# Kernel optimization log

Measured on AMD Instinct MI355X. Metric: run time of the kernel, lower is better.

The kernel has to match this reference:

```python
import jax, jax.numpy as jnp
import numpy as np

D_MODEL = 2048
N_HEADS = 32
N_KV_HEADS = 8
HEAD_DIM = D_MODEL // N_HEADS
ROPE_BASE = 10000.0

def setup_inputs() -> dict:
    key = jax.random.key(0)
    ks = jax.random.split(key, 5)
    B, S = 1, 2048
    x = jax.random.normal(ks[0], (B, S, D_MODEL), dtype=jnp.float32)
    sc = 1.0 / np.sqrt(D_MODEL)
    Wq = jax.random.normal(ks[1], (D_MODEL, D_MODEL), dtype=jnp.float32) * sc
    Wk = jax.random.normal(ks[2], (N_KV_HEADS * HEAD_DIM, D_MODEL), dtype=jnp.float32) * sc
    Wv = jax.random.normal(ks[3], (N_KV_HEADS * HEAD_DIM, D_MODEL), dtype=jnp.float32) * sc
    Wo = jax.random.normal(ks[4], (D_MODEL, D_MODEL), dtype=jnp.float32) * sc
    return {"x": x, "Wq": Wq, "Wk": Wk, "Wv": Wv, "Wo": Wo}

def _rope_cos_sin(seq_len, dtype):
    inv_freq = 1.0 / (ROPE_BASE ** (jnp.arange(0, HEAD_DIM, 2, dtype=jnp.float32) / HEAD_DIM))
    t = jnp.arange(seq_len, dtype=jnp.float32)
    freqs = jnp.einsum('i,j->ij', t, inv_freq)          # [S, hd/2]
    emb = jnp.concatenate([freqs, freqs], axis=-1)      # [S, hd]
    return jnp.cos(emb).astype(dtype), jnp.sin(emb).astype(dtype)

def _rotate_half(x):
    x1, x2 = x[..., : HEAD_DIM // 2], x[..., HEAD_DIM // 2 :]
    return jnp.concatenate([-x2, x1], axis=-1)

def reference(x, Wq, Wk, Wv, Wo):
    B, S, _ = x.shape
    scale = HEAD_DIM ** -0.5
    # projections (Linear: x @ W.T)
    q = (x @ Wq.T).reshape(B, S, N_HEADS, HEAD_DIM).transpose(0, 2, 1, 3)      # [B,H,S,hd]
    k = (x @ Wk.T).reshape(B, S, N_KV_HEADS, HEAD_DIM).transpose(0, 2, 1, 3)   # [B,Hkv,S,hd]
    v = (x @ Wv.T).reshape(B, S, N_KV_HEADS, HEAD_DIM).transpose(0, 2, 1, 3)
    cos, sin = _rope_cos_sin(S, x.dtype)                # [S,hd], broadcasts over B,H
    q = q * cos + _rotate_half(q) * sin
    k = k * cos + _rotate_half(k) * sin
    rep = N_HEADS // N_KV_HEADS
    k = jnp.repeat(k, rep, axis=1)                       # [B,H,S,hd]
    v = jnp.repeat(v, rep, axis=1)
    scores = jnp.einsum('bhqd,bhkd->bhqk', q, k) * scale # [B,H,S,S]
    attn = jax.nn.softmax(scores, axis=-1)
    out = jnp.einsum('bhqk,bhkd->bhqd', attn, v)         # [B,H,S,hd]
    out = out.transpose(0, 2, 1, 3).reshape(B, S, D_MODEL)
    return out @ Wo.T
```

## Files before the change

### kernel.cpp

```cpp
#include <hip/hip_runtime.h>
#include <hip/hip_bf16.h>
#include <cmath>

typedef __bf16 bf16_t;
typedef __attribute__((ext_vector_type(8))) __bf16 bf16x8;
typedef __attribute__((ext_vector_type(4))) float f32x4;
typedef __attribute__((ext_vector_type(4))) short s16x4;

#define S_LEN 2048
#define DMODEL 2048
#define KVDIM 512
#define NHEADS 32
#define NKV 8
#define HDIM 64

__device__ inline f32x4 zero4() { f32x4 z; z[0]=0.f; z[1]=0.f; z[2]=0.f; z[3]=0.f; return z; }

__global__ void convert_all(const float* __restrict__ s0, bf16_t* __restrict__ d0,
                            const float* __restrict__ s1, bf16_t* __restrict__ d1,
                            const float* __restrict__ s2, bf16_t* __restrict__ d2,
                            const float* __restrict__ s3, bf16_t* __restrict__ d3,
                            const float* __restrict__ s4, bf16_t* __restrict__ d4) {
  int b = blockIdx.x;
  const float* src; bf16_t* dst; int boff;
  if      (b < 2048) { src = s0; dst = d0; boff = b; }
  else if (b < 4096) { src = s1; dst = d1; boff = b - 2048; }
  else if (b < 4608) { src = s2; dst = d2; boff = b - 4096; }
  else if (b < 5120) { src = s3; dst = d3; boff = b - 4608; }
  else               { src = s4; dst = d4; boff = b - 5120; }
  int idx = (boff * 256 + threadIdx.x) * 8;
  bf16x8 v;
#pragma unroll
  for (int j = 0; j < 8; j++) v[j] = (bf16_t)src[idx + j];
  *(bf16x8*)(dst + idx) = v;
}

template <int BN, bool F32OUT>
__device__ __forceinline__ void gemm_core(const bf16_t* __restrict__ A,
                                          const bf16_t* __restrict__ Bt,
                                          void* __restrict__ Cout,
                                          int N, int K, int bm, int bn) {
  constexpr int NT_W = BN / 32;
  __shared__ __attribute__((aligned(16))) bf16_t As[128 * 64];
  __shared__ __attribute__((aligned(16))) bf16_t Bs[BN * 64];
  const int tid  = threadIdx.x;
  const int wave = tid >> 6, lane = tid & 63;
  const int wm = wave >> 1, wn = wave & 1;
  const int quad = lane >> 4, lr = lane & 15;
  const int srow = lane >> 3, scol = lane & 7;

  f32x4 acc[4][NT_W];
#pragma unroll
  for (int i = 0; i < 4; i++)
#pragma unroll
    for (int j = 0; j < NT_W; j++) acc[i][j] = zero4();

  for (int k0 = 0; k0 < K; k0 += 64) {
#pragma unroll
    for (int i = 0; i < 4; i++) {
      const bf16_t* gA = A + (size_t)(bm + i * 32 + wave * 8 + srow) * K + k0 + scol * 8;
      bf16_t* lA = As + (i * 32 + wave * 8) * 64;
      __builtin_amdgcn_global_load_lds((const __attribute__((address_space(1))) void*)gA,
                                       (__attribute__((address_space(3))) void*)lA, 16, 0, 0);
    }
#pragma unroll
    for (int i = 0; i < BN / 32; i++) {
      const bf16_t* gB = Bt + (size_t)(bn + i * 32 + wave * 8 + srow) * K + k0 + scol * 8;
      bf16_t* lB = Bs + (i * 32 + wave * 8) * 64;
      __builtin_amdgcn_global_load_lds((const __attribute__((address_space(1))) void*)gB,
                                       (__attribute__((address_space(3))) void*)lB, 16, 0, 0);
    }
    __syncthreads();
#pragma unroll
    for (int ks = 0; ks < 2; ks++) {
      bf16x8 a[4], b[NT_W];
#pragma unroll
      for (int mt = 0; mt < 4; mt++)
        a[mt] = *(const bf16x8*)&As[(wm * 64 + mt * 16 + lr) * 64 + ks * 32 + quad * 8];
#pragma unroll
      for (int nt = 0; nt < NT_W; nt++)
        b[nt] = *(const bf16x8*)&Bs[(wn * (BN / 2) + nt * 16 + lr) * 64 + ks * 32 + quad * 8];
#pragma unroll
      for (int mt = 0; mt < 4; mt++)
#pragma unroll
        for (int nt = 0; nt < NT_W; nt++)
          acc[mt][nt] = __builtin_amdgcn_mfma_f32_16x16x32_bf16(a[mt], b[nt], acc[mt][nt], 0, 0, 0);
    }
    __syncthreads();
  }

#pragma unroll
  for (int mt = 0; mt < 4; mt++)
#pragma unroll
    for (int nt = 0; nt < NT_W; nt++)
#pragma unroll
      for (int r = 0; r < 4; r++) {
        int row = bm + wm * 64 + mt * 16 + quad * 4 + r;
        int col = bn + wn * (BN / 2) + nt * 16 + lr;
        if (F32OUT) ((float*)Cout)[(size_t)row * N + col] = acc[mt][nt][r];
        else ((bf16_t*)Cout)[(size_t)row * N + col] = (bf16_t)acc[mt][nt][r];
      }
}

__global__ __launch_bounds__(256) void gemm_proj(const bf16_t* __restrict__ xb,
                                                 const bf16_t* __restrict__ Wqb,
                                                 const bf16_t* __restrict__ Wkb,
                                                 const bf16_t* __restrict__ Wvb,
                                                 bf16_t* __restrict__ qb,
                                                 bf16_t* __restrict__ kb,
                                                 bf16_t* __restrict__ vb) {
  int b = blockIdx.x;
  if (b < 512) {
    gemm_core<64, false>(xb, Wqb, qb, 2048, 2048, (b >> 5) * 128, (b & 31) * 64);
  } else if (b < 640) {
    int r = b - 512;
    gemm_core<64, false>(xb, Wkb, kb, 512, 2048, (r >> 3) * 128, (r & 7) * 64);
  } else {
    int r = b - 640;
    gemm_core<64, false>(Wvb, xb, vb, 2048, 2048, (r >> 5) * 128, (r & 31) * 64);
  }
}

__global__ __launch_bounds__(256) void gemm_out(const bf16_t* __restrict__ A,
                                                const bf16_t* __restrict__ Bt,
                                                float* __restrict__ C) {
  int b = blockIdx.x;
  gemm_core<64, true>(A, Bt, C, 2048, 2048, (b >> 5) * 128, (b & 31) * 64);
}

__global__ void rope_k(bf16_t* __restrict__ kb) {
  int idx = blockIdx.x * 256 + threadIdx.x;
  int s = idx >> 8;
  int rem = idx & 255;
  int head = rem >> 5;
  int i = rem & 31;
  float freq = __expf(-0.2878231366f * (float)i);
  float ang = (float)s * freq;
  float sn, cs;
  sincosf(ang, &sn, &cs);
  size_t base = (size_t)s * KVDIM + head * 64 + i;
  float x0 = (float)kb[base];
  float x1 = (float)kb[base + 32];
  kb[base]      = (bf16_t)(x0 * cs - x1 * sn);
  kb[base + 32] = (bf16_t)(x1 * cs + x0 * sn);
}

__global__ __launch_bounds__(256) void attn_kernel(const bf16_t* __restrict__ q,
                                                   const bf16_t* __restrict__ k,
                                                   const bf16_t* __restrict__ vT,
                                                   bf16_t* __restrict__ out) {
  __shared__ __attribute__((aligned(16))) bf16_t Ks[128 * 64];
  __shared__ __attribute__((aligned(16))) bf16_t Vs[64 * 128];
  const int tid  = threadIdx.x;
  const int wave = tid >> 6, lane = tid & 63;
  const int quad = lane >> 4, lr = lane & 15;
  const int srow = lane >> 3, scol = lane & 7;
  const int vrow = lane >> 4, vcol = lane & 15;
  const int cg = scol ^ srow;
  const int qt = blockIdx.x, h = blockIdx.y;
  const int hkv = h >> 2;
  const int qrow0 = qt * 64 + wave * 16;
  const int sw = lr & 7;
  const int c0 = (quad ^ sw) * 8;
  const int c1 = ((quad + 4) ^ sw) * 8;

  bf16x8 aq0, aq1;
  {
    const bf16_t* qp = q + (size_t)(qrow0 + lr) * DMODEL + h * HDIM + quad * 8;
    bf16x8 r0 = *(const bf16x8*)qp;
    bf16x8 r1 = *(const bf16x8*)(qp + 32);
    float srow_f = (float)(qrow0 + lr);
#pragma unroll
    for (int j = 0; j < 8; j++) {
      float freq = __expf(-0.2878231366f * (float)(quad * 8 + j));
      float sn, cs;
      sincosf(srow_f * freq, &sn, &cs);
      float x0 = (float)r0[j], x1 = (float)r1[j];
      aq0[j] = (bf16_t)(x0 * cs - x1 * sn);
      aq1[j] = (bf16_t)(x1 * cs + x0 * sn);
    }
  }

  f32x4 O[4];
  float l_lane = 0.f;
#pragma unroll
  for (int mt = 0; mt < 4; mt++) O[mt] = zero4();

  for (int kt = 0; kt < S_LEN; kt += 128) {
#pragma unroll
    for (int j = 0; j < 4; j++) {
      const bf16_t* gK = k + (size_t)(kt + wave * 32 + j * 8 + srow) * KVDIM + hkv * HDIM + cg * 8;
      bf16_t* lK = Ks + (wave * 32 + j * 8) * 64;
      __builtin_amdgcn_global_load_lds((const __attribute__((address_space(1))) void*)gK,
                                       (__attribute__((address_space(3))) void*)lK, 16, 0, 0);
    }
#pragma unroll
    for (int j = 0; j < 4; j++) {
      int dg = wave * 16 + j * 4 + vrow;
      int cgv = vcol ^ (dg & 7);
      const bf16_t* gV = vT + (size_t)(hkv * HDIM + dg) * S_LEN + kt + cgv * 8;
      bf16_t* lV = Vs + (wave * 16 + j * 4) * 128;
      __builtin_amdgcn_global_load_lds((const __attribute__((address_space(1))) void*)gV,
                                       (__attribute__((address_space(3))) void*)lV, 16, 0, 0);
    }
    __syncthreads();

    f32x4 sc[8];
#pragma unroll
    for (int nt = 0; nt < 8; nt++) sc[nt] = zero4();
#pragma unroll
    for (int nt = 0; nt < 8; nt++) {
      const int rk = (nt * 16 + lr) * 64;
      bf16x8 kb0 = *(const bf16x8*)&Ks[rk + c0];
      bf16x8 kb1 = *(const bf16x8*)&Ks[rk + c1];
      sc[nt] = __builtin_amdgcn_mfma_f32_16x16x32_bf16(kb0, aq0, sc[nt], 0, 0, 0);
      sc[nt] = __builtin_amdgcn_mfma_f32_16x16x32_bf16(kb1, aq1, sc[nt], 0, 0, 0);
    }
    s16x4 bp[8];
#pragma unroll
    for (int nt = 0; nt < 8; nt++) {
#pragma unroll
      for (int r = 0; r < 4; r++) {
        float p = __expf(sc[nt][r] * 0.125f);
        l_lane += p;
        bf16_t pb = (bf16_t)p;
        bp[nt][r] = __builtin_bit_cast(short, pb);
      }
    }
#pragma unroll
    for (int nt = 0; nt < 8; nt++) {
      const int slot = ((nt * 2 + (quad >> 1)) ^ sw) * 8 + (quad & 1) * 4;
      s16x4 av[4];
#pragma unroll
      for (int mt = 0; mt < 4; mt++)
        av[mt] = *(const s16x4*)&Vs[(mt * 16 + lr) * 128 + slot];
#pragma unroll
      for (int mt = 0; mt < 4; mt++)
        O[mt] = __builtin_amdgcn_mfma_f32_16x16x16bf16_1k(av[mt], bp[nt], O[mt], 0, 0, 0);
    }
    __syncthreads();
  }

  l_lane += __shfl_xor(l_lane, 16);
  l_lane += __shfl_xor(l_lane, 32);
  float inv_l = 1.f / l_lane;

#pragma unroll
  for (int mt = 0; mt < 4; mt++) {
    s16x4 ov;
#pragma unroll
    for (int r = 0; r < 4; r++) {
      bf16_t b = (bf16_t)(O[mt][r] * inv_l);
      ov[r] = __builtin_bit_cast(short, b);
    }
    *(s16x4*)&out[(size_t)(qrow0 + lr) * DMODEL + h * HDIM + mt * 16 + quad * 4] = ov;
  }
}

extern "C" void kernel_launch(void* const* d_in, const int* in_sizes, int n_in,
                              void* d_out, int out_size, void* d_ws, size_t ws_size,
                              hipStream_t stream) {
  (void)in_sizes; (void)n_in; (void)out_size; (void)ws_size;
  const float* x  = (const float*)d_in[0];
  const float* Wq = (const float*)d_in[1];
  const float* Wk = (const float*)d_in[2];
  const float* Wv = (const float*)d_in[3];
  const float* Wo = (const float*)d_in[4];

  bf16_t* xb  = (bf16_t*)d_ws;
  bf16_t* Wqb = xb  + (size_t)4 * 1024 * 1024;
  bf16_t* Wkb = Wqb + (size_t)4 * 1024 * 1024;
  bf16_t* Wvb = Wkb + (size_t)1024 * 1024;
  bf16_t* qb  = Wvb + (size_t)1024 * 1024;
  bf16_t* kb  = qb  + (size_t)4 * 1024 * 1024;
  bf16_t* vb  = kb  + (size_t)1024 * 1024;
  bf16_t* Wob = vb  + (size_t)1024 * 1024;
  bf16_t* ab  = xb;

  dim3 blk(256);
  convert_all<<<7168, blk, 0, stream>>>(x, xb, Wq, Wqb, Wk, Wkb, Wv, Wvb, Wo, Wob);
  gemm_proj<<<768, blk, 0, stream>>>(xb, Wqb, Wkb, Wvb, qb, kb, vb);
  rope_k<<<2048, blk, 0, stream>>>(kb);
  attn_kernel<<<dim3(S_LEN / 64, NHEADS), blk, 0, stream>>>(qb, kb, vb, ab);
  gemm_out<<<512, blk, 0, stream>>>(ab, Wob, (float*)d_out);
}
```

Before: 239.0 us.

## Process two 16-row query sets per wave in attention to reuse K/V fragments

```diff
diff --git a/kernel.cpp b/kernel.cpp
--- a/kernel.cpp
+++ b/kernel.cpp
@@ -159,32 +159,36 @@
   const int cg = scol ^ srow;
   const int qt = blockIdx.x, h = blockIdx.y;
   const int hkv = h >> 2;
-  const int qrow0 = qt * 64 + wave * 16;
+  const int qrow0 = qt * 128 + wave * 32;
   const int sw = lr & 7;
   const int c0 = (quad ^ sw) * 8;
   const int c1 = ((quad + 4) ^ sw) * 8;
 
-  bf16x8 aq0, aq1;
-  {
-    const bf16_t* qp = q + (size_t)(qrow0 + lr) * DMODEL + h * HDIM + quad * 8;
+  bf16x8 aqA0, aqA1, aqB0, aqB1;
+#pragma unroll
+  for (int set = 0; set < 2; set++) {
+    int row = qrow0 + set * 16 + lr;
+    const bf16_t* qp = q + (size_t)row * DMODEL + h * HDIM + quad * 8;
     bf16x8 r0 = *(const bf16x8*)qp;
     bf16x8 r1 = *(const bf16x8*)(qp + 32);
-    float srow_f = (float)(qrow0 + lr);
+    float srow_f = (float)row;
+    bf16x8 a0, a1;
 #pragma unroll
     for (int j = 0; j < 8; j++) {
       float freq = __expf(-0.2878231366f * (float)(quad * 8 + j));
       float sn, cs;
       sincosf(srow_f * freq, &sn, &cs);
       float x0 = (float)r0[j], x1 = (float)r1[j];
-      aq0[j] = (bf16_t)(x0 * cs - x1 * sn);
-      aq1[j] = (bf16_t)(x1 * cs + x0 * sn);
-    }
-  }
-
-  f32x4 O[4];
-  float l_lane = 0.f;
-#pragma unroll
-  for (int mt = 0; mt < 4; mt++) O[mt] = zero4();
+      a0[j] = (bf16_t)(x0 * cs - x1 * sn);
+      a1[j] = (bf16_t)(x1 * cs + x0 * sn);
+    }
+    if (set == 0) { aqA0 = a0; aqA1 = a1; } else { aqB0 = a0; aqB1 = a1; }
+  }
+
+  f32x4 OA[4], OB[4];
+  float lA = 0.f, lB = 0.f;
+#pragma unroll
+  for (int mt = 0; mt < 4; mt++) { OA[mt] = zero4(); OB[mt] = zero4(); }
 
   for (int kt = 0; kt < S_LEN; kt += 128) {
 #pragma unroll
@@ -205,26 +209,25 @@
     }
     __syncthreads();
 
-    f32x4 sc[8];
-#pragma unroll
-    for (int nt = 0; nt < 8; nt++) sc[nt] = zero4();
+    s16x4 bpA[8], bpB[8];
 #pragma unroll
     for (int nt = 0; nt < 8; nt++) {
       const int rk = (nt * 16 + lr) * 64;
       bf16x8 kb0 = *(const bf16x8*)&Ks[rk + c0];
       bf16x8 kb1 = *(const bf16x8*)&Ks[rk + c1];
-      sc[nt] = __builtin_amdgcn_mfma_f32_16x16x32_bf16(kb0, aq0, sc[nt], 0, 0, 0);
-      sc[nt] = __builtin_amdgcn_mfma_f32_16x16x32_bf16(kb1, aq1, sc[nt], 0, 0, 0);
-    }
-    s16x4 bp[8];
-#pragma unroll
-    for (int nt = 0; nt < 8; nt++) {
+      f32x4 sA = zero4(), sB = zero4();
+      sA = __builtin_amdgcn_mfma_f32_16x16x32_bf16(kb0, aqA0, sA, 0, 0, 0);
+      sA = __builtin_amdgcn_mfma_f32_16x16x32_bf16(kb1, aqA1, sA, 0, 0, 0);
+      sB = __builtin_amdgcn_mfma_f32_16x16x32_bf16(kb0, aqB0, sB, 0, 0, 0);
+      sB = __builtin_amdgcn_mfma_f32_16x16x32_bf16(kb1, aqB1, sB, 0, 0, 0);
 #pragma unroll
       for (int r = 0; r < 4; r++) {
-        float p = __expf(sc[nt][r] * 0.125f);
-        l_lane += p;
-        bf16_t pb = (bf16_t)p;
-        bp[nt][r] = __builtin_bit_cast(short, pb);
+        float pA = __expf(sA[r] * 0.125f);
+        lA += pA;
+        bpA[nt][r] = __builtin_bit_cast(short, (bf16_t)pA);
+        float pB = __expf(sB[r] * 0.125f);
+        lB += pB;
+        bpB[nt][r] = __builtin_bit_cast(short, (bf16_t)pB);
       }
     }
 #pragma unroll
@@ -235,25 +238,31 @@
       for (int mt = 0; mt < 4; mt++)
         av[mt] = *(const s16x4*)&Vs[(mt * 16 + lr) * 128 + slot];
 #pragma unroll
-      for (int mt = 0; mt < 4; mt++)
-        O[mt] = __builtin_amdgcn_mfma_f32_16x16x16bf16_1k(av[mt], bp[nt], O[mt], 0, 0, 0);
-    }
-    __syncthreads();
-  }
-
-  l_lane += __shfl_xor(l_lane, 16);
-  l_lane += __shfl_xor(l_lane, 32);
-  float inv_l = 1.f / l_lane;
+      for (int mt = 0; mt < 4; mt++) {
+        OA[mt] = __builtin_amdgcn_mfma_f32_16x16x16bf16_1k(av[mt], bpA[nt], OA[mt], 0, 0, 0);
+        OB[mt] = __builtin_amdgcn_mfma_f32_16x16x16bf16_1k(av[mt], bpB[nt], OB[mt], 0, 0, 0);
+      }
+    }
+    __syncthreads();
+  }
+
+  lA += __shfl_xor(lA, 16);
+  lA += __shfl_xor(lA, 32);
+  lB += __shfl_xor(lB, 16);
+  lB += __shfl_xor(lB, 32);
+  float invA = 1.f / lA;
+  float invB = 1.f / lB;
 
 #pragma unroll
   for (int mt = 0; mt < 4; mt++) {
-    s16x4 ov;
+    s16x4 ovA, ovB;
 #pragma unroll
     for (int r = 0; r < 4; r++) {
-      bf16_t b = (bf16_t)(O[mt][r] * inv_l);
-      ov[r] = __builtin_bit_cast(short, b);
-    }
-    *(s16x4*)&out[(size_t)(qrow0 + lr) * DMODEL + h * HDIM + mt * 16 + quad * 4] = ov;
+      ovA[r] = __builtin_bit_cast(short, (bf16_t)(OA[mt][r] * invA));
+      ovB[r] = __builtin_bit_cast(short, (bf16_t)(OB[mt][r] * invB));
+    }
+    *(s16x4*)&out[(size_t)(qrow0 + lr) * DMODEL + h * HDIM + mt * 16 + quad * 4] = ovA;
+    *(s16x4*)&out[(size_t)(qrow0 + 16 + lr) * DMODEL + h * HDIM + mt * 16 + quad * 4] = ovB;
   }
 }
 
@@ -281,6 +290,6 @@
   convert_all<<<7168, blk, 0, stream>>>(x, xb, Wq, Wqb, Wk, Wkb, Wv, Wvb, Wo, Wob);
   gemm_proj<<<768, blk, 0, stream>>>(xb, Wqb, Wkb, Wvb, qb, kb, vb);
   rope_k<<<2048, blk, 0, stream>>>(kb);
-  attn_kernel<<<dim3(S_LEN / 64, NHEADS), blk, 0, stream>>>(qb, kb, vb, ab);
+  attn_kernel<<<dim3(S_LEN / 128, NHEADS), blk, 0, stream>>>(qb, kb, vb, ab);
   gemm_out<<<512, blk, 0, stream>>>(ab, Wob, (float*)d_out);
 }
```

Result: no change. 237.6 us (-0.6%).
